# Kernel tuning notes

Hardware: AMD Instinct MI355X
Metric: run time of the kernel (lower is better)

The kernel has to match this reference:

```python
import jax, jax.numpy as jnp
import numpy as np
from jax import lax

B, C, H, W = 8, 36, 256, 256
E, K, TD = 6, 2, 32
HID = C * 2  # ffn_expansion_factor = 2
EPS = 1e-10


def _conv3x3(x, w):
    # x: [B, Cin, H, W], w: [Cout, Cin, 3, 3], stride 1, pad 1, no bias
    return lax.conv_general_dilated(
        x, w, window_strides=(1, 1), padding=[(1, 1), (1, 1)],
        dimension_numbers=("NCHW", "OIHW", "NCHW"))


def _cv_squared(v):
    # torch .var() is unbiased (ddof=1)
    return jnp.var(v, ddof=1) / (jnp.mean(v) ** 2 + EPS)


def setup_inputs() -> dict:
    key = jax.random.key(0)
    ks = jax.random.split(key, 10)
    s = 0.05
    return {
        "x": jax.random.normal(ks[0], (B, C, H, W), dtype=jnp.float32),
        "time": jax.random.normal(ks[1], (B, TD), dtype=jnp.float32),
        # FeatureWiseAffine: Linear(time_dim -> expert_dim*2)
        "time_w": jax.random.normal(ks[2], (TD, HID), dtype=jnp.float32) * s,
        "time_b": jnp.zeros((HID,), dtype=jnp.float32),
        # gate: Linear(72,72) -> LeakyReLU -> Linear(72,6)
        "gate_w1": jax.random.normal(ks[3], (HID, HID), dtype=jnp.float32) * s,
        "gate_b1": jnp.zeros((HID,), dtype=jnp.float32),
        "gate_w2": jax.random.normal(ks[4], (HID, E), dtype=jnp.float32) * s,
        "gate_b2": jnp.zeros((E,), dtype=jnp.float32),
        # per-expert conv weights, stacked over experts
        "conv1_w": jax.random.normal(ks[5], (E, HID, C, 3, 3), dtype=jnp.float32) * s,
        "conv2_w": jax.random.normal(ks[6], (E, C, HID, 3, 3), dtype=jnp.float32) * s,
    }


def reference(x, time, time_w, time_b, gate_w1, gate_b1, gate_w2, gate_b2,
              conv1_w, conv2_w):
    # ---- gating (eval mode: no noise) ----
    # NOTE: source names are swapped: self.maxpool = AdaptiveAvgPool2d(1),
    # self.meanpool = AdaptiveMaxPool2d(1). Order preserved: [avg, max].
    avg_vec = jnp.mean(x, axis=(2, 3))              # [B, C]
    max_vec = jnp.max(x, axis=(2, 3))               # [B, C]
    v = jnp.concatenate([avg_vec, max_vec], axis=1)  # [B, 2C]
    v = v + time @ time_w + time_b                   # FeatureWiseAffine (additive)
    h = v @ gate_w1 + gate_b1
    h = jnp.where(h > 0, h, 0.01 * h)                # LeakyReLU(0.01)
    clean_logits = h @ gate_w2 + gate_b2             # [B, E]

    top_vals, top_idx = lax.top_k(clean_logits, min(K + 1, E))
    topk_gates = jax.nn.softmax(top_vals[:, :K], axis=1)     # [B, K]
    rows = jnp.arange(B)[:, None]
    gates = jnp.zeros_like(clean_logits).at[rows, top_idx[:, :K]].set(topk_gates)

    importance = gates.sum(axis=0)                           # [E]
    load = (gates > 0).sum(axis=0).astype(jnp.float32)       # [E] (eval path)
    loss = (_cv_squared(importance) + _cv_squared(load)) * 0.01

    # ---- dense equivalent of sparse dispatch / expert / gate-weighted combine ----
    # y[b] = sum_e gates[b,e] * expert_e(x[b]); zero gates contribute nothing,
    # identical to SparseDispatcher's gather -> conv -> scatter-add combine.
    y = jnp.zeros_like(x)
    for e in range(E):
        t = _conv3x3(x, conv1_w[e])
        t = jax.nn.gelu(t, approximate=False)   # F.gelu default = exact erf
        t = _conv3x3(t, conv2_w[e])
        y = y + gates[:, e].reshape(B, 1, 1, 1) * t
    return y, loss
```

## Files before the change

kernel.cpp:

```cpp
#include <hip/hip_runtime.h>
#include <math.h>

#define BB 8
#define CCH 36
#define HH 256
#define WW 256
#define EE 6
#define TDIM 32
#define HID 72
#define WS_GATES (BB*CCH*2)
#define WT1_OFF 4096
#define WT2_OFF (4096 + 368640)

#define TW 16
#define TH 8
#define XR 12
#define XC 20
#define CIP 40
#define TR 10
#define TC 18

typedef __attribute__((ext_vector_type(8))) short bf16x8;
typedef __attribute__((ext_vector_type(4))) float f32x4;
typedef __attribute__((ext_vector_type(4))) short short4v;

static __device__ __forceinline__ unsigned short f2bf(float f) {
  union { float f; unsigned u; } v; v.f = f;
  unsigned r = v.u + 0x7FFF + ((v.u >> 16) & 1);
  return (unsigned short)(r >> 16);
}
static __device__ __forceinline__ float gelu_fast(float x) {
  float u2 = x * (1.5957691216f + 0.0713548162f * x * x);
  u2 = fminf(fmaxf(u2, -30.f), 30.f);
  float e = __expf(u2);
  return x * e * __builtin_amdgcn_rcpf(e + 1.f);
}

__global__ __launch_bounds__(256) void pool_kernel(const float* __restrict__ x,
                                                   float* __restrict__ ws) {
  const int bc = blockIdx.x;
  const float* p = x + (size_t)bc * (HH * WW);
  float s = 0.f, m = -INFINITY;
  for (int i = threadIdx.x; i < (HH * WW) / 4; i += 256) {
    float4 v = ((const float4*)p)[i];
    s += v.x + v.y + v.z + v.w;
    m = fmaxf(m, fmaxf(fmaxf(v.x, v.y), fmaxf(v.z, v.w)));
  }
  for (int off = 32; off; off >>= 1) {
    s += __shfl_down(s, off);
    m = fmaxf(m, __shfl_down(m, off));
  }
  __shared__ float ss[4], sm[4];
  int wid = threadIdx.x >> 6, lane = threadIdx.x & 63;
  if (lane == 0) { ss[wid] = s; sm[wid] = m; }
  __syncthreads();
  if (threadIdx.x == 0) {
    float S = ss[0] + ss[1] + ss[2] + ss[3];
    float M = fmaxf(fmaxf(sm[0], sm[1]), fmaxf(sm[2], sm[3]));
    ws[bc] = S * (1.f / (HH * WW));
    ws[BB * CCH + bc] = M;
  }
}

__global__ void gate_kernel(const float* __restrict__ time,
                            const float* __restrict__ time_w,
                            const float* __restrict__ time_b,
                            const float* __restrict__ w1, const float* __restrict__ b1,
                            const float* __restrict__ w2, const float* __restrict__ b2,
                            float* __restrict__ ws, float* __restrict__ loss_out) {
  __shared__ float v[BB * HID];
  __shared__ float h[BB * HID];
  __shared__ float logits[BB * EE];
  const int t = threadIdx.x;
  const float* avg = ws;
  const float* mx = ws + BB * CCH;
  for (int i = t; i < BB * HID; i += blockDim.x) {
    int b = i / HID, c = i % HID;
    float base = (c < CCH) ? avg[b * CCH + c] : mx[b * CCH + (c - CCH)];
    float acc = time_b[c];
    for (int k = 0; k < TDIM; k++) acc += time[b * TDIM + k] * time_w[k * HID + c];
    v[i] = base + acc;
  }
  __syncthreads();
  for (int i = t; i < BB * HID; i += blockDim.x) {
    int b = i / HID, c = i % HID;
    float acc = b1[c];
    for (int k = 0; k < HID; k++) acc += v[b * HID + k] * w1[k * HID + c];
    h[i] = acc > 0.f ? acc : 0.01f * acc;
  }
  __syncthreads();
  for (int i = t; i < BB * EE; i += blockDim.x) {
    int b = i / EE, e = i % EE;
    float acc = b2[e];
    for (int k = 0; k < HID; k++) acc += h[b * HID + k] * w2[k * EE + e];
    logits[i] = acc;
  }
  __syncthreads();
  if (t == 0) {
    float imp[EE], ld[EE];
    for (int e = 0; e < EE; e++) { imp[e] = 0.f; ld[e] = 0.f; }
    for (int b = 0; b < BB; b++) {
      int i1 = -1, i2 = -1;
      float v1 = -1e30f, v2 = -1e30f;
      for (int e = 0; e < EE; e++) {
        float lv = logits[b * EE + e];
        if (lv > v1) { v2 = v1; i2 = i1; v1 = lv; i1 = e; }
        else if (lv > v2) { v2 = lv; i2 = e; }
      }
      float e2 = expf(v2 - v1);
      float g1 = 1.f / (1.f + e2), g2 = e2 / (1.f + e2);
      for (int e = 0; e < EE; e++) ws[WS_GATES + b * EE + e] = 0.f;
      ws[WS_GATES + b * EE + i1] = g1;
      ws[WS_GATES + b * EE + i2] = g2;
      imp[i1] += g1; imp[i2] += g2;
      ld[i1] += 1.f; ld[i2] += 1.f;
    }
    float loss = 0.f;
    {
      float m = 0.f; for (int e = 0; e < EE; e++) m += imp[e]; m /= EE;
      float var = 0.f; for (int e = 0; e < EE; e++) { float d = imp[e] - m; var += d * d; }
      var /= (EE - 1);
      loss += var / (m * m + 1e-10f);
      m = 0.f; for (int e = 0; e < EE; e++) m += ld[e]; m /= EE;
      var = 0.f; for (int e = 0; e < EE; e++) { float d = ld[e] - m; var += d * d; }
      var /= (EE - 1);
      loss += var / (m * m + 1e-10f);
    }
    loss_out[0] = 0.01f * loss;
  }
}

__global__ __launch_bounds__(256) void wxform_kernel(const float* __restrict__ w1,
                                                     const float* __restrict__ w2,
                                                     unsigned short* __restrict__ wt1,
                                                     unsigned short* __restrict__ wt2) {
  int i = blockIdx.x * 256 + threadIdx.x;
  const int n1 = 360 * 512;
  if (i < n1) {
    int j = i & 7;
    int lane = (i >> 3) & 63;
    int f = i >> 9;
    int mt = f % 5;  f /= 5;
    int kc = f % 4;  f /= 4;
    int dx = f % 3;  int e = f / 3;
    int co = mt * 16 + (lane & 15);
    int k = kc * 32 + (lane >> 4) * 8 + j;
    int dy = k / 40, ci = k % 40;
    float v = 0.f;
    if (co < HID && k < 120 && ci < CCH)
      v = w1[(((size_t)(e * HID + co) * CCH + ci) * 3 + dy) * 3 + dx];
    wt1[i] = f2bf(v);
  }
  const int n2 = 378 * 512;
  if (i < n2) {
    int j = i & 7;
    int lane = (i >> 3) & 63;
    int f = i >> 9;
    int mt = f % 3;  f /= 3;
    int kc = f % 7;  f /= 7;
    int dx = f % 3;  int e = f / 3;
    int co = mt * 16 + (lane & 15);
    int k = kc * 32 + (lane >> 4) * 8 + j;
    int dy = k / 72, ci = k % 72;
    float v = 0.f;
    if (co < CCH && k < 216)
      v = w2[(((size_t)(e * CCH + co) * HID + ci) * 3 + dy) * 3 + dx];
    wt2[i] = f2bf(v);
  }
}

__global__ __launch_bounds__(256, 3) void conv_kernel(
    const float* __restrict__ x,
    const unsigned short* __restrict__ wt1,
    const unsigned short* __restrict__ wt2,
    const float* __restrict__ wsg,
    float* __restrict__ y) {
  __shared__ __align__(16) char lds[45120];
  char* xsB = lds;
  char* tsB = lds + 19200;

  const int tid = threadIdx.x;
  const int w = tid >> 6;
  const int lane = tid & 63;
  const int l15 = lane & 15;
  const int kl = lane >> 4;
  const int b = blockIdx.y;
  const int tileId = (blockIdx.x & 7) * 64 + (blockIdx.x >> 3);
  const int tx0 = (tileId & 15) * TW;
  const int ty0 = (tileId >> 4) * TH;
  const size_t xbase = (size_t)b * (CCH * HH * WW);

  int eids[2] = {0, 0};
  float gvals[2] = {0.f, 0.f};
  int ne = 0;
  for (int e = 0; e < EE; e++) {
    float g = wsg[b * EE + e];
    if (g != 0.f && ne < 2) { eids[ne] = e; gvals[ne] = g; ne++; }
  }

  if (tid < XR * XC) {
    const int xr = tid / XC, xc = tid - (tid / XC) * XC;
    const int gy = ty0 - 2 + xr, gx = tx0 - 2 + xc;
    const bool valid = ((unsigned)gy < (unsigned)HH) && ((unsigned)gx < (unsigned)WW);
    const float* xp = x + xbase + (size_t)(gy * WW + gx);
    char* dstb = xsB + 2 * ((xr * XC + xc) * CIP);
#pragma unroll
    for (int c4 = 0; c4 < 9; c4++) {
      short4v pk;
#pragma unroll
      for (int q = 0; q < 4; q++) {
        int ci = c4 * 4 + q;
        float v = valid ? xp[(size_t)ci << 16] : 0.f;
        ((short*)&pk)[q] = (short)f2bf(v);
      }
      *(short4v*)(dstb + c4 * 8) = pk;
    }
    *(short4v*)(dstb + 72) = (short4v){0, 0, 0, 0};
  }

  int xkoff[4];
#pragma unroll
  for (int kc = 0; kc < 4; kc++) {
    int k0 = kc * 32 + kl * 8;
    int d = (k0 >= 80) ? 2 : (k0 >= 40 ? 1 : 0);
    xkoff[kc] = (k0 < 120) ? (d * (XC * CIP) + (k0 - 40 * d)) * 2 : -1;
  }
  int tkoff[7];
#pragma unroll
  for (int kc = 0; kc < 7; kc++) {
    int k0 = kc * 32 + kl * 8;
    int d = (k0 >= 144) ? 2 : (k0 >= 72 ? 1 : 0);
    tkoff[kc] = (k0 < 216) ? (d * (TC * HID) + (k0 - 72 * d)) * 2 : -1;
  }

  int pbase1[3], tsoff[3], vimg[3], pst[3];
#pragma unroll
  for (int i = 0; i < 3; i++) {
    int p = (w + 4 * i) * 16 + l15;
    int tr = p / TC, tc = p - tr * TC;
    pst[i] = (p < TR * TC) ? 1 : 0;
    int trc = tr < (TR - 1) ? tr : (TR - 1);
    pbase1[i] = (trc * XC + tc) * (CIP * 2);
    tsoff[i] = ((trc * TC + tc) * HID) * 2;
    int gy = ty0 - 1 + tr, gx = tx0 - 1 + tc;
    vimg[i] = (pst[i] && (unsigned)gy < (unsigned)HH && (unsigned)gx < (unsigned)WW) ? 1 : 0;
  }
  int pbase2[2];
#pragma unroll
  for (int i = 0; i < 2; i++) pbase2[i] = (((w + 4 * i) * TC) + l15) * (HID * 2);

  const unsigned short* w1lane = wt1 + lane * 8;
  const unsigned short* w2lane = wt2 + lane * 8;

  f32x4 yacc[2][3];
#pragma unroll
  for (int i = 0; i < 2; i++)
#pragma unroll
    for (int mt = 0; mt < 3; mt++) yacc[i][mt] = (f32x4){0.f, 0.f, 0.f, 0.f};

  __syncthreads();

#pragma unroll
  for (int ei = 0; ei < 2; ei++) {
    if (ei >= ne) break;
    const float gv = gvals[ei];
    const unsigned short* w1p = w1lane + eids[ei] * 30720;
    const unsigned short* w2p = w2lane + eids[ei] * 32256;

    f32x4 acc[3][5];
#pragma unroll
    for (int i = 0; i < 3; i++)
#pragma unroll
      for (int mt = 0; mt < 5; mt++) acc[i][mt] = (f32x4){0.f, 0.f, 0.f, 0.f};

    bf16x8 aA[5], aB[5];
#pragma unroll
    for (int mt = 0; mt < 5; mt++) aA[mt] = *(const bf16x8*)(w1p + mt * 512);

#pragma unroll
    for (int jj = 0; jj < 12; jj++) {
      if (jj < 11) {
#pragma unroll
        for (int mt = 0; mt < 5; mt++)
          ((jj & 1) ? aA : aB)[mt] = *(const bf16x8*)(w1p + ((jj + 1) * 5 + mt) * 512);
      }
      const int kc = jj & 3;
      const int dxo = (jj >> 2) * (CIP * 2);
      bf16x8 bv[3];
#pragma unroll
      for (int i = 0; i < 3; i++) {
        int ba = (xkoff[kc] >= 0) ? (pbase1[i] + xkoff[kc] + dxo) : 0;
        bv[i] = *(const bf16x8*)(xsB + ba);
      }
      __builtin_amdgcn_s_setprio(1);
#pragma unroll
      for (int mt = 0; mt < 5; mt++) {
        bf16x8 av = ((jj & 1) ? aB : aA)[mt];
#pragma unroll
        for (int i = 0; i < 3; i++)
          acc[i][mt] = __builtin_amdgcn_mfma_f32_16x16x32_bf16(av, bv[i], acc[i][mt], 0, 0, 0);
      }
      __builtin_amdgcn_s_setprio(0);
    }

    bf16x8 cA[3], cB[3];
#pragma unroll
    for (int mt = 0; mt < 3; mt++) cA[mt] = *(const bf16x8*)(w2p + mt * 512);

#pragma unroll
    for (int i = 0; i < 3; i++) {
      if (pst[i]) {
#pragma unroll
        for (int mt = 0; mt < 5; mt++) {
          int co0 = mt * 16 + kl * 4;
          if (co0 < HID) {
            short4v pk;
            float v0 = vimg[i] ? gelu_fast(acc[i][mt].x) : 0.f;
            float v1 = vimg[i] ? gelu_fast(acc[i][mt].y) : 0.f;
            float v2 = vimg[i] ? gelu_fast(acc[i][mt].z) : 0.f;
            float v3 = vimg[i] ? gelu_fast(acc[i][mt].w) : 0.f;
            pk.x = (short)f2bf(v0); pk.y = (short)f2bf(v1);
            pk.z = (short)f2bf(v2); pk.w = (short)f2bf(v3);
            *(short4v*)(tsB + tsoff[i] + co0 * 2) = pk;
          }
        }
      }
    }
    __syncthreads();

    f32x4 acc2[2][3];
#pragma unroll
    for (int i = 0; i < 2; i++)
#pragma unroll
      for (int mt = 0; mt < 3; mt++) acc2[i][mt] = (f32x4){0.f, 0.f, 0.f, 0.f};

#pragma unroll
    for (int jj = 0; jj < 21; jj++) {
      if (jj < 20) {
#pragma unroll
        for (int mt = 0; mt < 3; mt++)
          ((jj & 1) ? cA : cB)[mt] = *(const bf16x8*)(w2p + ((jj + 1) * 3 + mt) * 512);
      }
      const int kc = jj % 7;
      const int dxo = (jj / 7) * (HID * 2);
      bf16x8 bv[2];
#pragma unroll
      for (int i = 0; i < 2; i++) {
        int ba = (tkoff[kc] >= 0) ? (pbase2[i] + tkoff[kc] + dxo) : 0;
        bv[i] = *(const bf16x8*)(tsB + ba);
      }
      __builtin_amdgcn_s_setprio(1);
#pragma unroll
      for (int mt = 0; mt < 3; mt++) {
        bf16x8 av = ((jj & 1) ? cB : cA)[mt];
#pragma unroll
        for (int i = 0; i < 2; i++)
          acc2[i][mt] = __builtin_amdgcn_mfma_f32_16x16x32_bf16(av, bv[i], acc2[i][mt], 0, 0, 0);
      }
      __builtin_amdgcn_s_setprio(0);
    }
#pragma unroll
    for (int i = 0; i < 2; i++)
#pragma unroll
      for (int mt = 0; mt < 3; mt++) yacc[i][mt] += gv * acc2[i][mt];
    __syncthreads();
  }

#pragma unroll
  for (int i = 0; i < 2; i++) {
    int row = w + 4 * i;
#pragma unroll
    for (int mt = 0; mt < 3; mt++) {
#pragma unroll
      for (int r = 0; r < 4; r++) {
        int co = mt * 16 + kl * 4 + r;
        if (co < CCH) {
          float v = (r == 0) ? yacc[i][mt].x : (r == 1) ? yacc[i][mt].y
                  : (r == 2) ? yacc[i][mt].z : yacc[i][mt].w;
          y[xbase + ((size_t)co << 16) + (size_t)((ty0 + row) * WW + tx0 + l15)] = v;
        }
      }
    }
  }
}

extern "C" void kernel_launch(void* const* d_in, const int* in_sizes, int n_in,
                              void* d_out, int out_size, void* d_ws, size_t ws_size,
                              hipStream_t stream) {
  const float* x      = (const float*)d_in[0];
  const float* time   = (const float*)d_in[1];
  const float* time_w = (const float*)d_in[2];
  const float* time_b = (const float*)d_in[3];
  const float* gw1    = (const float*)d_in[4];
  const float* gb1    = (const float*)d_in[5];
  const float* gw2    = (const float*)d_in[6];
  const float* gb2    = (const float*)d_in[7];
  const float* w1     = (const float*)d_in[8];
  const float* w2     = (const float*)d_in[9];
  float* out = (float*)d_out;
  float* ws  = (float*)d_ws;
  unsigned short* wt1 = (unsigned short*)((char*)d_ws + WT1_OFF);
  unsigned short* wt2 = (unsigned short*)((char*)d_ws + WT2_OFF);

  hipLaunchKernelGGL(pool_kernel, dim3(BB * CCH), dim3(256), 0, stream, x, ws);
  hipLaunchKernelGGL(gate_kernel, dim3(1), dim3(128), 0, stream,
                     time, time_w, time_b, gw1, gb1, gw2, gb2,
                     ws, out + (size_t)(out_size - 1));
  hipLaunchKernelGGL(wxform_kernel, dim3(756), dim3(256), 0, stream, w1, w2, wt1, wt2);
  hipLaunchKernelGGL(conv_kernel, dim3(512, BB), dim3(256), 0, stream,
                     x, wt1, wt2, ws + WS_GATES, out);
}
```

Baseline: 251.6 us.

## Use channel-blocked LDS layout, merge pool and weight-transform kernels

Changes the LDS layout of the input tile and the GELU intermediate from pixel-major with padded channels to channel-block-major, with 8 channels (16 bytes) per pixel per block. The fragment loads become conflict-free 16-byte reads without the negative-offset guards. The pool and weight-transform kernels are merged into one launch to save a launch, and GELU and bf16 conversion use cheaper formulations. The GELU form drops the clamp, which relies on rcp handling inf correctly, and the bf16 conversion now goes through the library intrinsic.

Measured after the change: 243.2 us. 3.3% less time.

```diff
diff --git a/kernel.cpp b/kernel.cpp
--- a/kernel.cpp
+++ b/kernel.cpp
@@ -1,4 +1,5 @@
 #include <hip/hip_runtime.h>
+#include <hip/hip_bf16.h>
 #include <math.h>
 
 #define BB 8
@@ -16,49 +17,85 @@
 #define TH 8
 #define XR 12
 #define XC 20
-#define CIP 40
 #define TR 10
 #define TC 18
 
 typedef __attribute__((ext_vector_type(8))) short bf16x8;
 typedef __attribute__((ext_vector_type(4))) float f32x4;
-typedef __attribute__((ext_vector_type(4))) short short4v;
 
 static __device__ __forceinline__ unsigned short f2bf(float f) {
-  union { float f; unsigned u; } v; v.f = f;
-  unsigned r = v.u + 0x7FFF + ((v.u >> 16) & 1);
-  return (unsigned short)(r >> 16);
+  __hip_bfloat16 h = __float2bfloat16(f);
+  return *(unsigned short*)&h;
 }
 static __device__ __forceinline__ float gelu_fast(float x) {
-  float u2 = x * (1.5957691216f + 0.0713548162f * x * x);
-  u2 = fminf(fmaxf(u2, -30.f), 30.f);
-  float e = __expf(u2);
-  return x * e * __builtin_amdgcn_rcpf(e + 1.f);
-}
-
-__global__ __launch_bounds__(256) void pool_kernel(const float* __restrict__ x,
-                                                   float* __restrict__ ws) {
-  const int bc = blockIdx.x;
-  const float* p = x + (size_t)bc * (HH * WW);
-  float s = 0.f, m = -INFINITY;
-  for (int i = threadIdx.x; i < (HH * WW) / 4; i += 256) {
-    float4 v = ((const float4*)p)[i];
-    s += v.x + v.y + v.z + v.w;
-    m = fmaxf(m, fmaxf(fmaxf(v.x, v.y), fmaxf(v.z, v.w)));
-  }
-  for (int off = 32; off; off >>= 1) {
-    s += __shfl_down(s, off);
-    m = fmaxf(m, __shfl_down(m, off));
-  }
-  __shared__ float ss[4], sm[4];
-  int wid = threadIdx.x >> 6, lane = threadIdx.x & 63;
-  if (lane == 0) { ss[wid] = s; sm[wid] = m; }
-  __syncthreads();
-  if (threadIdx.x == 0) {
-    float S = ss[0] + ss[1] + ss[2] + ss[3];
-    float M = fmaxf(fmaxf(sm[0], sm[1]), fmaxf(sm[2], sm[3]));
-    ws[bc] = S * (1.f / (HH * WW));
-    ws[BB * CCH + bc] = M;
+  float n2u = x * (-1.5957691216f - 0.0713548162f * x * x);
+  float r = __builtin_amdgcn_rcpf(1.f + __expf(n2u));
+  return x * r;
+}
+
+__global__ __launch_bounds__(256) void poolwx_kernel(const float* __restrict__ x,
+                                                     const float* __restrict__ w1,
+                                                     const float* __restrict__ w2,
+                                                     float* __restrict__ ws,
+                                                     unsigned short* __restrict__ wt1,
+                                                     unsigned short* __restrict__ wt2) {
+  if (blockIdx.x < 288) {
+    const int bc = blockIdx.x;
+    const float* p = x + (size_t)bc * (HH * WW);
+    float s = 0.f, m = -INFINITY;
+    for (int i = threadIdx.x; i < (HH * WW) / 4; i += 256) {
+      float4 v = ((const float4*)p)[i];
+      s += v.x + v.y + v.z + v.w;
+      m = fmaxf(m, fmaxf(fmaxf(v.x, v.y), fmaxf(v.z, v.w)));
+    }
+    for (int off = 32; off; off >>= 1) {
+      s += __shfl_down(s, off);
+      m = fmaxf(m, __shfl_down(m, off));
+    }
+    __shared__ float ss[4], sm[4];
+    int wid = threadIdx.x >> 6, lane = threadIdx.x & 63;
+    if (lane == 0) { ss[wid] = s; sm[wid] = m; }
+    __syncthreads();
+    if (threadIdx.x == 0) {
+      float S = ss[0] + ss[1] + ss[2] + ss[3];
+      float M = fmaxf(fmaxf(sm[0], sm[1]), fmaxf(sm[2], sm[3]));
+      ws[bc] = S * (1.f / (HH * WW));
+      ws[BB * CCH + bc] = M;
+    }
+    return;
+  }
+  int i = (blockIdx.x - 288) * 256 + threadIdx.x;
+  const int n1 = 360 * 512;
+  if (i < n1) {
+    int j = i & 7;
+    int lane = (i >> 3) & 63;
+    int f = i >> 9;
+    int mt = f % 5;  f /= 5;
+    int kc = f % 4;  f /= 4;
+    int dx = f % 3;  int e = f / 3;
+    int co = mt * 16 + (lane & 15);
+    int k = kc * 32 + (lane >> 4) * 8 + j;
+    int dy = k / 40, ci = k % 40;
+    float v = 0.f;
+    if (co < HID && k < 120 && ci < CCH)
+      v = w1[(((size_t)(e * HID + co) * CCH + ci) * 3 + dy) * 3 + dx];
+    wt1[i] = f2bf(v);
+  }
+  const int n2 = 378 * 512;
+  if (i < n2) {
+    int j = i & 7;
+    int lane = (i >> 3) & 63;
+    int f = i >> 9;
+    int mt = f % 3;  f /= 3;
+    int kc = f % 7;  f /= 7;
+    int dx = f % 3;  int e = f / 3;
+    int co = mt * 16 + (lane & 15);
+    int k = kc * 32 + (lane >> 4) * 8 + j;
+    int dy = k / 72, ci = k % 72;
+    float v = 0.f;
+    if (co < CCH && k < 216)
+      v = w2[(((size_t)(e * CCH + co) * HID + ci) * 3 + dy) * 3 + dx];
+    wt2[i] = f2bf(v);
   }
 }
 
@@ -130,45 +167,6 @@
   }
 }
 
-__global__ __launch_bounds__(256) void wxform_kernel(const float* __restrict__ w1,
-                                                     const float* __restrict__ w2,
-                                                     unsigned short* __restrict__ wt1,
-                                                     unsigned short* __restrict__ wt2) {
-  int i = blockIdx.x * 256 + threadIdx.x;
-  const int n1 = 360 * 512;
-  if (i < n1) {
-    int j = i & 7;
-    int lane = (i >> 3) & 63;
-    int f = i >> 9;
-    int mt = f % 5;  f /= 5;
-    int kc = f % 4;  f /= 4;
-    int dx = f % 3;  int e = f / 3;
-    int co = mt * 16 + (lane & 15);
-    int k = kc * 32 + (lane >> 4) * 8 + j;
-    int dy = k / 40, ci = k % 40;
-    float v = 0.f;
-    if (co < HID && k < 120 && ci < CCH)
-      v = w1[(((size_t)(e * HID + co) * CCH + ci) * 3 + dy) * 3 + dx];
-    wt1[i] = f2bf(v);
-  }
-  const int n2 = 378 * 512;
-  if (i < n2) {
-    int j = i & 7;
-    int lane = (i >> 3) & 63;
-    int f = i >> 9;
-    int mt = f % 3;  f /= 3;
-    int kc = f % 7;  f /= 7;
-    int dx = f % 3;  int e = f / 3;
-    int co = mt * 16 + (lane & 15);
-    int k = kc * 32 + (lane >> 4) * 8 + j;
-    int dy = k / 72, ci = k % 72;
-    float v = 0.f;
-    if (co < CCH && k < 216)
-      v = w2[(((size_t)(e * CCH + co) * HID + ci) * 3 + dy) * 3 + dx];
-    wt2[i] = f2bf(v);
-  }
-}
-
 __global__ __launch_bounds__(256, 3) void conv_kernel(
     const float* __restrict__ x,
     const unsigned short* __restrict__ wt1,
@@ -203,34 +201,36 @@
     const int gy = ty0 - 2 + xr, gx = tx0 - 2 + xc;
     const bool valid = ((unsigned)gy < (unsigned)HH) && ((unsigned)gx < (unsigned)WW);
     const float* xp = x + xbase + (size_t)(gy * WW + gx);
-    char* dstb = xsB + 2 * ((xr * XC + xc) * CIP);
-#pragma unroll
-    for (int c4 = 0; c4 < 9; c4++) {
-      short4v pk;
+    char* dstb = xsB + (xr * XC + xc) * 16;
+#pragma unroll
+    for (int c8 = 0; c8 < 5; c8++) {
+      unsigned int pk[4];
 #pragma unroll
       for (int q = 0; q < 4; q++) {
-        int ci = c4 * 4 + q;
-        float v = valid ? xp[(size_t)ci << 16] : 0.f;
-        ((short*)&pk)[q] = (short)f2bf(v);
-      }
-      *(short4v*)(dstb + c4 * 8) = pk;
-    }
-    *(short4v*)(dstb + 72) = (short4v){0, 0, 0, 0};
-  }
-
-  int xkoff[4];
+        int ci0 = c8 * 8 + q * 2, ci1 = ci0 + 1;
+        float v0 = (ci0 < CCH && valid) ? xp[(size_t)ci0 << 16] : 0.f;
+        float v1 = (ci1 < CCH && valid) ? xp[(size_t)ci1 << 16] : 0.f;
+        pk[q] = (unsigned)f2bf(v0) | ((unsigned)f2bf(v1) << 16);
+      }
+      *(uint4*)(dstb + c8 * 3840) = make_uint4(pk[0], pk[1], pk[2], pk[3]);
+    }
+  }
+
+  int xkc[4];
 #pragma unroll
   for (int kc = 0; kc < 4; kc++) {
     int k0 = kc * 32 + kl * 8;
     int d = (k0 >= 80) ? 2 : (k0 >= 40 ? 1 : 0);
-    xkoff[kc] = (k0 < 120) ? (d * (XC * CIP) + (k0 - 40 * d)) * 2 : -1;
-  }
-  int tkoff[7];
+    int ci0 = k0 - 40 * d;
+    xkc[kc] = (k0 < 120) ? ((ci0 >> 3) * 3840 + d * 320) : 0;
+  }
+  int tkc[7];
 #pragma unroll
   for (int kc = 0; kc < 7; kc++) {
     int k0 = kc * 32 + kl * 8;
     int d = (k0 >= 144) ? 2 : (k0 >= 72 ? 1 : 0);
-    tkoff[kc] = (k0 < 216) ? (d * (TC * HID) + (k0 - 72 * d)) * 2 : -1;
+    int ci0 = k0 - 72 * d;
+    tkc[kc] = (k0 < 216) ? ((ci0 >> 3) * 2880 + d * 288) : 0;
   }
 
   int pbase1[3], tsoff[3], vimg[3], pst[3];
@@ -240,14 +240,14 @@
     int tr = p / TC, tc = p - tr * TC;
     pst[i] = (p < TR * TC) ? 1 : 0;
     int trc = tr < (TR - 1) ? tr : (TR - 1);
-    pbase1[i] = (trc * XC + tc) * (CIP * 2);
-    tsoff[i] = ((trc * TC + tc) * HID) * 2;
+    pbase1[i] = trc * 320 + tc * 16;
+    tsoff[i] = trc * 288 + tc * 16;
     int gy = ty0 - 1 + tr, gx = tx0 - 1 + tc;
     vimg[i] = (pst[i] && (unsigned)gy < (unsigned)HH && (unsigned)gx < (unsigned)WW) ? 1 : 0;
   }
   int pbase2[2];
 #pragma unroll
-  for (int i = 0; i < 2; i++) pbase2[i] = (((w + 4 * i) * TC) + l15) * (HID * 2);
+  for (int i = 0; i < 2; i++) pbase2[i] = (w + 4 * i) * 288 + l15 * 16;
 
   const unsigned short* w1lane = wt1 + lane * 8;
   const unsigned short* w2lane = wt2 + lane * 8;
@@ -285,13 +285,11 @@
           ((jj & 1) ? aA : aB)[mt] = *(const bf16x8*)(w1p + ((jj + 1) * 5 + mt) * 512);
       }
       const int kc = jj & 3;
-      const int dxo = (jj >> 2) * (CIP * 2);
+      const int dxo = (jj >> 2) * 16;
       bf16x8 bv[3];
 #pragma unroll
-      for (int i = 0; i < 3; i++) {
-        int ba = (xkoff[kc] >= 0) ? (pbase1[i] + xkoff[kc] + dxo) : 0;
-        bv[i] = *(const bf16x8*)(xsB + ba);
-      }
+      for (int i = 0; i < 3; i++)
+        bv[i] = *(const bf16x8*)(xsB + (pbase1[i] + xkc[kc] + dxo));
       __builtin_amdgcn_s_setprio(1);
 #pragma unroll
       for (int mt = 0; mt < 5; mt++) {
@@ -314,14 +312,14 @@
         for (int mt = 0; mt < 5; mt++) {
           int co0 = mt * 16 + kl * 4;
           if (co0 < HID) {
-            short4v pk;
             float v0 = vimg[i] ? gelu_fast(acc[i][mt].x) : 0.f;
             float v1 = vimg[i] ? gelu_fast(acc[i][mt].y) : 0.f;
             float v2 = vimg[i] ? gelu_fast(acc[i][mt].z) : 0.f;
             float v3 = vimg[i] ? gelu_fast(acc[i][mt].w) : 0.f;
-            pk.x = (short)f2bf(v0); pk.y = (short)f2bf(v1);
-            pk.z = (short)f2bf(v2); pk.w = (short)f2bf(v3);
-            *(short4v*)(tsB + tsoff[i] + co0 * 2) = pk;
+            unsigned int lo = (unsigned)f2bf(v0) | ((unsigned)f2bf(v1) << 16);
+            unsigned int hi = (unsigned)f2bf(v2) | ((unsigned)f2bf(v3) << 16);
+            int addr = (co0 >> 3) * 2880 + tsoff[i] + (co0 & 7) * 2;
+            *(uint2*)(tsB + addr) = make_uint2(lo, hi);
           }
         }
       }
@@ -342,13 +340,11 @@
           ((jj & 1) ? cA : cB)[mt] = *(const bf16x8*)(w2p + ((jj + 1) * 3 + mt) * 512);
       }
       const int kc = jj % 7;
-      const int dxo = (jj / 7) * (HID * 2);
+      const int dxo = (jj / 7) * 16;
       bf16x8 bv[2];
 #pragma unroll
-      for (int i = 0; i < 2; i++) {
-        int ba = (tkoff[kc] >= 0) ? (pbase2[i] + tkoff[kc] + dxo) : 0;
-        bv[i] = *(const bf16x8*)(tsB + ba);
-      }
+      for (int i = 0; i < 2; i++)
+        bv[i] = *(const bf16x8*)(tsB + (pbase2[i] + tkc[kc] + dxo));
       __builtin_amdgcn_s_setprio(1);
 #pragma unroll
       for (int mt = 0; mt < 3; mt++) {
@@ -402,11 +398,11 @@
   unsigned short* wt1 = (unsigned short*)((char*)d_ws + WT1_OFF);
   unsigned short* wt2 = (unsigned short*)((char*)d_ws + WT2_OFF);
 
-  hipLaunchKernelGGL(pool_kernel, dim3(BB * CCH), dim3(256), 0, stream, x, ws);
+  hipLaunchKernelGGL(poolwx_kernel, dim3(288 + 756), dim3(256), 0, stream,
+                     x, w1, w2, ws, wt1, wt2);
   hipLaunchKernelGGL(gate_kernel, dim3(1), dim3(128), 0, stream,
                      time, time_w, time_b, gw1, gb1, gw2, gb2,
                      ws, out + (size_t)(out_size - 1));
-  hipLaunchKernelGGL(wxform_kernel, dim3(756), dim3(256), 0, stream, w1, w2, wt1, wt2);
   hipLaunchKernelGGL(conv_kernel, dim3(512, BB), dim3(256), 0, stream,
                      x, wt1, wt2, ws + WS_GATES, out);
 }
```
